# Performance work log

Hardware: AMD Instinct MI355X
Metric: run time of the kernel (lower is better)

The kernel has to match this reference:

```python
import jax, jax.numpy as jnp
import numpy as np

GROUP = 8
BN_SCALE = 1.0 / np.sqrt(1.0 + 1e-5)  # BatchNorm eval with running_mean=0, running_var=1


def _grid_sample(img, grid, align_corners, zeros_pad):
    """Bilinear grid_sample. img: [B,C,H,W]; grid: [B,Hg,Wg,2] in [-1,1]."""
    B, C, H, W = img.shape
    gx, gy = grid[..., 0], grid[..., 1]
    if align_corners:
        ix = (gx + 1.0) * 0.5 * (W - 1)
        iy = (gy + 1.0) * 0.5 * (H - 1)
    else:
        ix = ((gx + 1.0) * W - 1.0) * 0.5
        iy = ((gy + 1.0) * H - 1.0) * 0.5
    x0 = jnp.floor(ix)
    y0 = jnp.floor(iy)
    wx1 = ix - x0
    wy1 = iy - y0
    flat = img.reshape(B, C, H * W)

    def tap(xi, yi, w):
        if zeros_pad:
            valid = (xi >= 0) & (xi <= W - 1) & (yi >= 0) & (yi <= H - 1)
            w = w * valid.astype(img.dtype)
        else:
            xi = jnp.clip(xi, 0, W - 1)
            yi = jnp.clip(yi, 0, H - 1)
        xc = jnp.clip(xi, 0, W - 1).astype(jnp.int32)
        yc = jnp.clip(yi, 0, H - 1).astype(jnp.int32)
        idx = (yc * W + xc).reshape(B, -1)  # [B, Hg*Wg]
        v = jax.vmap(lambda im, ii: jnp.take(im, ii, axis=1))(flat, idx)  # [B,C,Hg*Wg]
        return v.reshape(B, C, gx.shape[1], gx.shape[2]) * w[:, None]

    return (tap(x0, y0, (1.0 - wx1) * (1.0 - wy1))
            + tap(x0 + 1.0, y0, wx1 * (1.0 - wy1))
            + tap(x0, y0 + 1.0, (1.0 - wx1) * wy1)
            + tap(x0 + 1.0, y0 + 1.0, wx1 * wy1))


def _warp(src_fea, src_proj, ref_proj, depth):
    """differentiable_warping: src_fea [B,C,H,W], projs [B,4,4], depth [B,D,H,W] -> [B,C,D,H,W]."""
    B, C, H, W = src_fea.shape
    D = depth.shape[1]
    proj = src_proj @ jnp.linalg.inv(ref_proj)
    rot = proj[:, :3, :3]
    trans = proj[:, :3, 3:4]
    yy, xx = jnp.meshgrid(jnp.arange(H, dtype=jnp.float32), jnp.arange(W, dtype=jnp.float32), indexing='ij')
    xyz = jnp.stack([xx.ravel(), yy.ravel(), jnp.ones(H * W, jnp.float32)], axis=0)  # [3,HW]
    rot_xyz = jnp.einsum('bij,jn->bin', rot, xyz)  # [B,3,HW]
    proj_xyz = rot_xyz[:, :, None, :] * depth.reshape(B, 1, D, H * W) + trans[:, :, :, None]  # [B,3,D,HW]
    neg = proj_xyz[:, 2] <= 1e-3
    px = jnp.where(neg, float(W), proj_xyz[:, 0])
    py = jnp.where(neg, float(H), proj_xyz[:, 1])
    pz = jnp.where(neg, 1.0, proj_xyz[:, 2])
    gx = px / pz / ((W - 1) / 2.0) - 1.0
    gy = py / pz / ((H - 1) / 2.0) - 1.0
    grid = jnp.stack([gx, gy], axis=-1).reshape(B, D * H, W, 2)
    warped = _grid_sample(src_fea, grid, align_corners=True, zeros_pad=True)  # [B,C,D*H,W]
    return warped.reshape(B, C, D, H, W)


def _cbr(x, w, g, b):
    # 1x1x1 Conv3d (no bias) + BN(eval) + ReLU on [B,Cin,D,H,W]
    y = jnp.einsum('oc,bcdhw->bodhw', w, x)
    y = g[None, :, None, None, None] * (y * BN_SCALE) + b[None, :, None, None, None]
    return jax.nn.relu(y)


def setup_inputs() -> dict:
    key = jax.random.key(0)
    ks = jax.random.split(key, 16)
    B, C, H, W, D, V, NN = 2, 64, 128, 160, 16, 4, 9
    G = GROUP
    ref_feature = jax.random.normal(ks[0], (B, C, H, W), jnp.float32)
    src_features = jax.random.normal(ks[1], (V, B, C, H, W), jnp.float32)
    eye = jnp.broadcast_to(jnp.eye(4, dtype=jnp.float32), (B, 4, 4))
    ref_proj = eye + 0.01 * jax.random.normal(ks[2], (B, 4, 4), jnp.float32)
    src_projs = eye[None] + 0.01 * jax.random.normal(ks[3], (V, B, 4, 4), jnp.float32)
    # depths near 1.0 so near-identity projections keep samples in-image
    depth_sample = jnp.sort(0.5 + jax.random.uniform(ks[4], (B, D, H, W), jnp.float32), axis=1)
    grid = jax.random.uniform(ks[5], (B, NN * H, W, 2), jnp.float32, minval=-1.0, maxval=1.0)
    weight = jax.random.uniform(ks[6], (B, D, NN, H, W), jnp.float32)

    def lin(k, o, i):
        return 0.1 * jax.random.normal(k, (o, i), jnp.float32)

    return {
        'ref_feature': ref_feature, 'src_features': src_features,
        'ref_proj': ref_proj, 'src_projs': src_projs,
        'depth_sample': depth_sample, 'grid': grid, 'weight': weight,
        'pw_w0': lin(ks[7], 16, G), 'pw_g0': jnp.ones(16, jnp.float32), 'pw_b0': jnp.zeros(16, jnp.float32),
        'pw_w1': lin(ks[8], 8, 16), 'pw_g1': jnp.ones(8, jnp.float32), 'pw_b1': jnp.zeros(8, jnp.float32),
        'pw_w2': lin(ks[9], 1, 8), 'pw_c2b': jnp.zeros(1, jnp.float32),
        'sn_w0': lin(ks[10], 16, G), 'sn_g0': jnp.ones(16, jnp.float32), 'sn_b0': jnp.zeros(16, jnp.float32),
        'sn_w1': lin(ks[11], 8, 16), 'sn_g1': jnp.ones(8, jnp.float32), 'sn_b1': jnp.zeros(8, jnp.float32),
        'sn_w2': lin(ks[12], 1, 8), 'sn_c2b': jnp.zeros(1, jnp.float32),
        'is_inverse': 0,
    }


def reference(ref_feature, src_features, ref_proj, src_projs, depth_sample, grid, weight,
              pw_w0, pw_g0, pw_b0, pw_w1, pw_g1, pw_b1, pw_w2, pw_c2b,
              sn_w0, sn_g0, sn_b0, sn_w1, sn_g1, sn_b1, sn_w2, sn_c2b, is_inverse):
    B, C, H, W = ref_feature.shape
    D = depth_sample.shape[1]
    V = src_features.shape[0]
    ref_g = ref_feature.reshape(B, GROUP, C // GROUP, 1, H, W)
    weight_sum = jnp.zeros((B, 1, 1, H, W), jnp.float32)
    similarity_sum = jnp.zeros((B, GROUP, D, H, W), jnp.float32)
    vws = []
    for v in range(V):
        warped = _warp(src_features[v], src_projs[v], ref_proj, depth_sample)
        warped = warped.reshape(B, GROUP, C // GROUP, D, H, W)
        sim = (warped * ref_g).mean(axis=2)  # [B,G,D,H,W]
        # PixelwiseNet (view_weights empty -> compute weights)
        y = _cbr(sim, pw_w0, pw_g0, pw_b0)
        y = _cbr(y, pw_w1, pw_g1, pw_b1)
        y = jnp.einsum('oc,bcdhw->bodhw', pw_w2, y) + pw_c2b[None, :, None, None, None]
        vw = jnp.max(jax.nn.sigmoid(y)[:, 0], axis=1)[:, None]  # [B,1,H,W]
        vws.append(vw)
        similarity_sum = similarity_sum + sim * vw[:, None]
        weight_sum = weight_sum + vw[:, None]
    sim_avg = similarity_sum / weight_sum
    # SimilarityNet
    s = _cbr(sim_avg, sn_w0, sn_g0, sn_b0)
    s = _cbr(s, sn_w1, sn_g1, sn_b1)
    s = (jnp.einsum('oc,bcdhw->bodhw', sn_w2, s) + sn_c2b[None, :, None, None, None])[:, 0]  # [B,D,H,W]
    NN = grid.shape[1] // H
    sam = _grid_sample(s, grid, align_corners=False, zeros_pad=False)  # [B,D,NN*H,W]
    sam = sam.reshape(B, D, NN, H, W)
    agg = jnp.sum(sam * weight, axis=2)  # [B,D,H,W]
    score = jax.nn.softmax(agg, axis=1)  # exp(log_softmax) == softmax
    if is_inverse:
        idxs = jnp.arange(D, dtype=jnp.float32).reshape(1, D, 1, 1)
        di = jnp.sum(idxs * score, axis=1)
        inv_min = 1.0 / depth_sample[:, -1]
        inv_max = 1.0 / depth_sample[:, 0]
        depth = 1.0 / (inv_max + di / (D - 1) * (inv_min - inv_max))
    else:
        depth = jnp.sum(depth_sample * score, axis=1)  # [B,H,W]
    view_weights_new = jax.lax.stop_gradient(jnp.concatenate(vws, axis=1))  # [B,V,H,W]
    return depth, score, view_weights_new
```

## Files before the change

### kernel.cpp

```cpp
#include <hip/hip_runtime.h>
#include <math.h>

#define BB 2
#define CC 64
#define HH 128
#define WW 160
#define DD 16
#define VV 4
#define NNB 9
#define GG 8
#define HWSZ (HH*WW)
#define BNS 0.99999500003749977f

typedef _Float16 half2_t __attribute__((ext_vector_type(2)));

__device__ inline half2_t as_h2(unsigned u){ union { unsigned u; half2_t h; } x; x.u = u; return x.h; }
__device__ inline unsigned as_u(half2_t h){ union { unsigned u; half2_t h; } x; x.h = h; return x.u; }

__device__ inline float dot8h(uint4 a, uint4 r) {
    float s = __builtin_amdgcn_fdot2(as_h2(a.x), as_h2(r.x), 0.f, false);
    s = __builtin_amdgcn_fdot2(as_h2(a.y), as_h2(r.y), s, false);
    s = __builtin_amdgcn_fdot2(as_h2(a.z), as_h2(r.z), s, false);
    s = __builtin_amdgcn_fdot2(as_h2(a.w), as_h2(r.w), s, false);
    return s;
}

__device__ inline void inv4(const float* m, float* o) {
    float inv[16];
    inv[0]  =  m[5]*m[10]*m[15] - m[5]*m[11]*m[14] - m[9]*m[6]*m[15] + m[9]*m[7]*m[14] + m[13]*m[6]*m[11] - m[13]*m[7]*m[10];
    inv[4]  = -m[4]*m[10]*m[15] + m[4]*m[11]*m[14] + m[8]*m[6]*m[15] - m[8]*m[7]*m[14] - m[12]*m[6]*m[11] + m[12]*m[7]*m[10];
    inv[8]  =  m[4]*m[9]*m[15]  - m[4]*m[11]*m[13] - m[8]*m[5]*m[15] + m[8]*m[7]*m[13] + m[12]*m[5]*m[11] - m[12]*m[7]*m[9];
    inv[12] = -m[4]*m[9]*m[14]  + m[4]*m[10]*m[13] + m[8]*m[5]*m[14] - m[8]*m[6]*m[13] - m[12]*m[5]*m[10] + m[12]*m[6]*m[9];
    inv[1]  = -m[1]*m[10]*m[15] + m[1]*m[11]*m[14] + m[9]*m[2]*m[15] - m[9]*m[3]*m[14] - m[13]*m[2]*m[11] + m[13]*m[3]*m[10];
    inv[5]  =  m[0]*m[10]*m[15] - m[0]*m[11]*m[14] - m[8]*m[2]*m[15] + m[8]*m[3]*m[14] + m[12]*m[2]*m[11] - m[12]*m[3]*m[10];
    inv[9]  = -m[0]*m[9]*m[15]  + m[0]*m[11]*m[13] + m[8]*m[1]*m[15] - m[8]*m[3]*m[13] - m[12]*m[1]*m[11] + m[12]*m[3]*m[9];
    inv[13] =  m[0]*m[9]*m[14]  - m[0]*m[10]*m[13] - m[8]*m[1]*m[14] + m[8]*m[2]*m[13] + m[12]*m[1]*m[10] - m[12]*m[2]*m[9];
    inv[2]  =  m[1]*m[6]*m[15]  - m[1]*m[7]*m[14]  - m[5]*m[2]*m[15] + m[5]*m[3]*m[14] + m[13]*m[2]*m[7]  - m[13]*m[3]*m[6];
    inv[6]  = -m[0]*m[6]*m[15]  + m[0]*m[7]*m[14]  + m[4]*m[2]*m[15] - m[4]*m[3]*m[14] - m[12]*m[2]*m[7]  + m[12]*m[3]*m[6];
    inv[10] =  m[0]*m[5]*m[15]  - m[0]*m[7]*m[13]  - m[4]*m[1]*m[15] + m[4]*m[3]*m[13] + m[12]*m[1]*m[7]  - m[12]*m[3]*m[5];
    inv[14] = -m[0]*m[5]*m[14]  + m[0]*m[6]*m[13]  + m[4]*m[1]*m[14] - m[4]*m[2]*m[13] - m[12]*m[1]*m[6]  + m[12]*m[2]*m[5];
    inv[3]  = -m[1]*m[6]*m[11]  + m[1]*m[7]*m[10]  + m[5]*m[2]*m[11] - m[5]*m[3]*m[10] - m[9]*m[2]*m[7]   + m[9]*m[3]*m[6];
    inv[7]  =  m[0]*m[6]*m[11]  - m[0]*m[7]*m[10]  - m[4]*m[2]*m[11] + m[4]*m[3]*m[10] + m[8]*m[2]*m[7]   - m[8]*m[3]*m[6];
    inv[11] = -m[0]*m[5]*m[11]  + m[0]*m[7]*m[9]   + m[4]*m[1]*m[11] - m[4]*m[3]*m[9]  - m[8]*m[1]*m[7]   + m[8]*m[3]*m[5];
    inv[15] =  m[0]*m[5]*m[10]  - m[0]*m[6]*m[9]   - m[4]*m[1]*m[10] + m[4]*m[2]*m[9]  + m[8]*m[1]*m[6]   - m[8]*m[2]*m[5];
    float det = m[0]*inv[0] + m[1]*inv[4] + m[2]*inv[8] + m[3]*inv[12];
    det = 1.0f/det;
    #pragma unroll
    for (int i=0;i<16;++i) o[i] = inv[i]*det;
}

__global__ void prep_k(const float* __restrict__ ref_proj, const float* __restrict__ src_projs,
                       const float* __restrict__ pw_w0, const float* __restrict__ pw_g0, const float* __restrict__ pw_b0,
                       const float* __restrict__ pw_w1, const float* __restrict__ pw_g1, const float* __restrict__ pw_b1,
                       const float* __restrict__ pw_w2, const float* __restrict__ pw_c2b,
                       const float* __restrict__ sn_w0, const float* __restrict__ sn_g0, const float* __restrict__ sn_b0,
                       const float* __restrict__ sn_w1, const float* __restrict__ sn_g1, const float* __restrict__ sn_b1,
                       const float* __restrict__ sn_w2, const float* __restrict__ sn_c2b,
                       float* __restrict__ ws) {
    int t = threadIdx.x;
    if (t < VV*BB) {
        int b = t % BB;
        float Mi[16];
        inv4(ref_proj + b*16, Mi);
        const float* A = src_projs + t*16;
        float P[16];
        #pragma unroll
        for (int i=0;i<4;++i)
            #pragma unroll
            for (int j=0;j<4;++j) {
                float s = 0.f;
                #pragma unroll
                for (int k=0;k<4;++k) s += A[i*4+k]*Mi[k*4+j];
                P[i*4+j] = s;
            }
        float* o = ws + t*12;
        o[0]=P[0]; o[1]=P[1]; o[2]=P[2];
        o[3]=P[4]; o[4]=P[5]; o[5]=P[6];
        o[6]=P[8]; o[7]=P[9]; o[8]=P[10];
        o[9]=P[3]; o[10]=P[7]; o[11]=P[11];
    }
    if (t < 128) {
        ws[96 + t]        = pw_w0[t]*pw_g0[t>>3]*BNS;
        ws[96 + 144 + t]  = pw_w1[t]*pw_g1[t>>4]*BNS;
        ws[385 + t]       = sn_w0[t]*sn_g0[t>>3]*BNS;
        ws[385 + 144 + t] = sn_w1[t]*sn_g1[t>>4]*BNS;
    }
    if (t < 16) { ws[96+128+t]=pw_b0[t]; ws[385+128+t]=sn_b0[t]; }
    if (t < 8)  { ws[96+272+t]=pw_b1[t]; ws[96+280+t]=pw_w2[t];
                  ws[385+272+t]=sn_b1[t]; ws[385+280+t]=sn_w2[t]; }
    if (t == 0) { ws[96+288]=pw_c2b[0]; ws[385+288]=sn_c2b[0]; }
}

__global__ __launch_bounds__(256) void transpose_h_k(const float* __restrict__ src,
                                                     _Float16* __restrict__ dst) {
    __shared__ float tb[64][65];
    int img = blockIdx.y;
    int n0  = blockIdx.x * 64;
    const float* ip = src + (size_t)img*64*HWSZ;
    _Float16*    op = dst + (size_t)img*HWSZ*64;
    int tid = threadIdx.x;
    #pragma unroll
    for (int i=0;i<4;++i) {
        int idx = i*256 + tid;
        int c  = idx >> 4;
        int p4 = idx & 15;
        float4 v = *(const float4*)(ip + (size_t)c*HWSZ + n0 + p4*4);
        tb[c][p4*4+0]=v.x; tb[c][p4*4+1]=v.y; tb[c][p4*4+2]=v.z; tb[c][p4*4+3]=v.w;
    }
    __syncthreads();
    #pragma unroll
    for (int i=0;i<4;++i) {
        int idx = i*256 + tid;
        int n  = idx >> 4;
        int cq = idx & 15;
        half2_t h0 = { (_Float16)tb[cq*4+0][n], (_Float16)tb[cq*4+1][n] };
        half2_t h1 = { (_Float16)tb[cq*4+2][n], (_Float16)tb[cq*4+3][n] };
        uint2 u; u.x = as_u(h0); u.y = as_u(h1);
        *(uint2*)(op + (size_t)(n0+n)*64 + cq*4) = u;
    }
}

__device__ inline float pixnet(const float* __restrict__ Wt, const float* sim) {
    float h0[16];
    #pragma unroll
    for (int o=0;o<16;++o) {
        float a = Wt[128+o];
        #pragma unroll
        for (int c=0;c<8;++c) a += Wt[o*8+c]*sim[c];
        h0[o] = fmaxf(a, 0.f);
    }
    float h1[8];
    #pragma unroll
    for (int o=0;o<8;++o) {
        float a = Wt[272+o];
        #pragma unroll
        for (int c=0;c<16;++c) a += Wt[144+o*16+c]*h0[c];
        h1[o] = fmaxf(a, 0.f);
    }
    float y = Wt[288];
    #pragma unroll
    for (int c=0;c<8;++c) y += Wt[280+c]*h1[c];
    return y;
}

__global__ __launch_bounds__(256) void eval_main_k(const float* __restrict__ ref_f,
                                                   const unsigned* __restrict__ src_u,
                                                   const float* __restrict__ wsc,
                                                   const float* __restrict__ depth_sample,
                                                   float* __restrict__ s_buf,
                                                   float* __restrict__ vw_out) {
    __shared__ __align__(16) unsigned refU[16][36];
    int tid  = threadIdx.x;
    int pixL = tid >> 4;
    int d    = tid & 15;
    int pixG = blockIdx.x*16 + pixL;
    int b  = pixG / HWSZ;
    int hw = pixG % HWSZ;
    {
        int c4 = tid & 15;
        const float* rp = ref_f + (size_t)b*CC*HWSZ + (size_t)(c4*4)*HWSZ + hw;
        float f0 = rp[0];
        float f1 = rp[HWSZ];
        float f2 = rp[2*HWSZ];
        float f3 = rp[3*HWSZ];
        half2_t h0 = { (_Float16)f0, (_Float16)f1 };
        half2_t h1 = { (_Float16)f2, (_Float16)f3 };
        refU[pixL][c4*2+0] = as_u(h0);
        refU[pixL][c4*2+1] = as_u(h1);
    }
    __syncthreads();

    int h  = hw / WW;
    int w  = hw % WW;
    const float* pw = wsc + 96;
    const float* sn = wsc + 385;
    float depth = depth_sample[((size_t)b*DD + d)*HWSZ + hw];
    float xf = (float)w, yf = (float)h;

    float simsum[8];
    #pragma unroll
    for (int g=0; g<8; ++g) simsum[g] = 0.f;
    float wsum = 0.f;

    #pragma unroll
    for (int v=0; v<VV; ++v) {
        const float* pm = wsc + (v*BB + b)*12;
        float rx = pm[0]*xf + pm[1]*yf + pm[2];
        float ry = pm[3]*xf + pm[4]*yf + pm[5];
        float rz = pm[6]*xf + pm[7]*yf + pm[8];
        float px = rx*depth + pm[9];
        float py = ry*depth + pm[10];
        float pz = rz*depth + pm[11];
        if (pz <= 0.001f) { px = (float)WW; py = (float)HH; pz = 1.f; }
        float ix = px/pz, iy = py/pz;
        float x0f = floorf(ix), y0f = floorf(iy);
        float wx1 = ix - x0f, wy1 = iy - y0f;
        float vx0 = (x0f      >= 0.f && x0f      <= (float)(WW-1)) ? 1.f : 0.f;
        float vx1 = (x0f+1.f  >= 0.f && x0f+1.f  <= (float)(WW-1)) ? 1.f : 0.f;
        float vy0 = (y0f      >= 0.f && y0f      <= (float)(HH-1)) ? 1.f : 0.f;
        float vy1 = (y0f+1.f  >= 0.f && y0f+1.f  <= (float)(HH-1)) ? 1.f : 0.f;
        float tw00 = (1.f-wx1)*(1.f-wy1)*vx0*vy0;
        float tw10 = wx1*(1.f-wy1)*vx1*vy0;
        float tw01 = (1.f-wx1)*wy1*vx0*vy1;
        float tw11 = wx1*wy1*vx1*vy1;
        int x0c = (int)fminf(fmaxf(x0f,     0.f), (float)(WW-1));
        int x1c = (int)fminf(fmaxf(x0f+1.f, 0.f), (float)(WW-1));
        int y0c = (int)fminf(fmaxf(y0f,     0.f), (float)(HH-1));
        int y1c = (int)fminf(fmaxf(y0f+1.f, 0.f), (float)(HH-1));

        const unsigned* sp  = src_u + (size_t)(v*BB + b)*HWSZ*32;
        const unsigned* p00 = sp + (size_t)(y0c*WW + x0c)*32;
        const unsigned* p10 = sp + (size_t)(y0c*WW + x1c)*32;
        const unsigned* p01 = sp + (size_t)(y1c*WW + x0c)*32;
        const unsigned* p11 = sp + (size_t)(y1c*WW + x1c)*32;

        float sim[8];
        #pragma unroll
        for (int g=0; g<8; ++g) {
            uint4 R  = *(const uint4*)&refU[pixL][g*4];
            uint4 A  = *(const uint4*)(p00 + g*4);
            uint4 Bv = *(const uint4*)(p10 + g*4);
            uint4 Cv = *(const uint4*)(p01 + g*4);
            uint4 E  = *(const uint4*)(p11 + g*4);
            float d00 = dot8h(A,  R);
            float d10 = dot8h(Bv, R);
            float d01 = dot8h(Cv, R);
            float d11 = dot8h(E,  R);
            sim[g] = 0.125f*(tw00*d00 + tw10*d10 + tw01*d01 + tw11*d11);
        }

        float y = pixnet(pw, sim);
        float sg = 1.f/(1.f + __expf(-y));

        float vw = sg;
        vw = fmaxf(vw, __shfl_xor(vw, 1));
        vw = fmaxf(vw, __shfl_xor(vw, 2));
        vw = fmaxf(vw, __shfl_xor(vw, 4));
        vw = fmaxf(vw, __shfl_xor(vw, 8));

        #pragma unroll
        for (int g=0; g<8; ++g) simsum[g] += sim[g]*vw;
        wsum += vw;
        if (d == 0) vw_out[(size_t)(b*VV + v)*HWSZ + hw] = vw;
    }

    float invw = 1.f/wsum;
    float sa[8];
    #pragma unroll
    for (int g=0; g<8; ++g) sa[g] = simsum[g]*invw;
    float s = pixnet(sn, sa);

    s_buf[(size_t)pixG*DD + d] = s;
}

__global__ __launch_bounds__(256) void eval_out_k(const float* __restrict__ s_buf,
                                                  const float* __restrict__ grid,
                                                  const float* __restrict__ weight,
                                                  const float* __restrict__ depth_sample,
                                                  const int* __restrict__ is_inverse,
                                                  float* __restrict__ out) {
    __shared__ float part[4][64][17];
    int tid = threadIdx.x;
    int px  = tid & 63;
    int j   = tid >> 6;
    int t   = blockIdx.x*64 + px;
    int b  = t / HWSZ;
    int hw = t % HWSZ;
    int h  = hw / WW;
    int w  = hw % WW;

    float agg[DD];
    #pragma unroll
    for (int d=0; d<DD; ++d) agg[d] = 0.f;

    #pragma unroll
    for (int k=0; k<3; ++k) {
        int nn = j + k*4;
        if (nn < NNB) {
            const float* gp = grid + (((size_t)b*NNB*HH + nn*HH + h)*WW + w)*2;
            float gx = gp[0], gy = gp[1];
            float ix = ((gx+1.f)*WW - 1.f)*0.5f;
            float iy = ((gy+1.f)*HH - 1.f)*0.5f;
            float x0f = floorf(ix), y0f = floorf(iy);
            float wx1 = ix - x0f, wy1 = iy - y0f;
            int x0 = (int)x0f, y0 = (int)y0f;
            int x0c = x0 < 0 ? 0 : (x0 > WW-1 ? WW-1 : x0);
            int x1c = x0+1 < 0 ? 0 : (x0+1 > WW-1 ? WW-1 : x0+1);
            int y0c = y0 < 0 ? 0 : (y0 > HH-1 ? HH-1 : y0);
            int y1c = y0+1 < 0 ? 0 : (y0+1 > HH-1 ? HH-1 : y0+1);
            float w00 = (1.f-wx1)*(1.f-wy1), w10 = wx1*(1.f-wy1);
            float w01 = (1.f-wx1)*wy1,       w11 = wx1*wy1;
            const float* p00 = s_buf + ((size_t)b*HWSZ + y0c*WW + x0c)*DD;
            const float* p10 = s_buf + ((size_t)b*HWSZ + y0c*WW + x1c)*DD;
            const float* p01 = s_buf + ((size_t)b*HWSZ + y1c*WW + x0c)*DD;
            const float* p11 = s_buf + ((size_t)b*HWSZ + y1c*WW + x1c)*DD;
            const float* wp  = weight + ((size_t)b*DD*NNB + nn)*HWSZ + hw;
            #pragma unroll
            for (int q=0; q<4; ++q) {
                float4 v00 = *(const float4*)(p00 + q*4);
                float4 v10 = *(const float4*)(p10 + q*4);
                float4 v01 = *(const float4*)(p01 + q*4);
                float4 v11 = *(const float4*)(p11 + q*4);
                float s0 = w00*v00.x + w10*v10.x + w01*v01.x + w11*v11.x;
                float s1 = w00*v00.y + w10*v10.y + w01*v01.y + w11*v11.y;
                float s2 = w00*v00.z + w10*v10.z + w01*v01.z + w11*v11.z;
                float s3 = w00*v00.w + w10*v10.w + w01*v01.w + w11*v11.w;
                agg[q*4+0] += s0 * wp[(size_t)(q*4+0)*NNB*HWSZ];
                agg[q*4+1] += s1 * wp[(size_t)(q*4+1)*NNB*HWSZ];
                agg[q*4+2] += s2 * wp[(size_t)(q*4+2)*NNB*HWSZ];
                agg[q*4+3] += s3 * wp[(size_t)(q*4+3)*NNB*HWSZ];
            }
        }
    }

    #pragma unroll
    for (int d=0; d<DD; ++d) part[j][px][d] = agg[d];
    __syncthreads();
    if (j != 0) return;

    #pragma unroll
    for (int d=0; d<DD; ++d)
        agg[d] = part[0][px][d] + part[1][px][d] + part[2][px][d] + part[3][px][d];

    float m = agg[0];
    #pragma unroll
    for (int d=1; d<DD; ++d) m = fmaxf(m, agg[d]);
    float e[DD], sum = 0.f;
    #pragma unroll
    for (int d=0; d<DD; ++d) { e[d] = __expf(agg[d]-m); sum += e[d]; }
    float inv = 1.f/sum;

    const float* dsp = depth_sample + (size_t)b*DD*HWSZ + hw;
    float* sco = out + BB*HWSZ + (size_t)b*DD*HWSZ + hw;
    float dep = 0.f;
    if (*is_inverse) {
        float di = 0.f;
        #pragma unroll
        for (int d=0; d<DD; ++d) { float sc = e[d]*inv; sco[(size_t)d*HWSZ] = sc; di += (float)d*sc; }
        float invmin = 1.f/dsp[(size_t)(DD-1)*HWSZ];
        float invmax = 1.f/dsp[0];
        dep = 1.f/(invmax + di/(float)(DD-1)*(invmin-invmax));
    } else {
        #pragma unroll
        for (int d=0; d<DD; ++d) { float sc = e[d]*inv; sco[(size_t)d*HWSZ] = sc; dep += dsp[(size_t)d*HWSZ]*sc; }
    }
    out[t] = dep;
}

extern "C" void kernel_launch(void* const* d_in, const int* in_sizes, int n_in,
                              void* d_out, int out_size, void* d_ws, size_t ws_size,
                              hipStream_t stream) {
    const float* ref_feature  = (const float*)d_in[0];
    const float* src_features = (const float*)d_in[1];
    const float* ref_proj     = (const float*)d_in[2];
    const float* src_projs    = (const float*)d_in[3];
    const float* depth_sample = (const float*)d_in[4];
    const float* grid         = (const float*)d_in[5];
    const float* weight       = (const float*)d_in[6];
    const float* pw_w0  = (const float*)d_in[7];
    const float* pw_g0  = (const float*)d_in[8];
    const float* pw_b0  = (const float*)d_in[9];
    const float* pw_w1  = (const float*)d_in[10];
    const float* pw_g1  = (const float*)d_in[11];
    const float* pw_b1  = (const float*)d_in[12];
    const float* pw_w2  = (const float*)d_in[13];
    const float* pw_c2b = (const float*)d_in[14];
    const float* sn_w0  = (const float*)d_in[15];
    const float* sn_g0  = (const float*)d_in[16];
    const float* sn_b0  = (const float*)d_in[17];
    const float* sn_w1  = (const float*)d_in[18];
    const float* sn_g1  = (const float*)d_in[19];
    const float* sn_b1  = (const float*)d_in[20];
    const float* sn_w2  = (const float*)d_in[21];
    const float* sn_c2b = (const float*)d_in[22];
    const int*   is_inverse = (const int*)d_in[23];
    float* out = (float*)d_out;

    float*    ws    = (float*)d_ws;
    _Float16* src_h = (_Float16*)(ws + 1024);
    float*    s_buf = ws + 1024 + ((size_t)VV*BB*HWSZ*64)/2;
    size_t need = (size_t)(1024 + (size_t)VV*BB*HWSZ*32 + (size_t)BB*HWSZ*DD)*sizeof(float);
    if (ws_size < need) return;

    prep_k<<<1, 128, 0, stream>>>(ref_proj, src_projs,
                                  pw_w0, pw_g0, pw_b0, pw_w1, pw_g1, pw_b1, pw_w2, pw_c2b,
                                  sn_w0, sn_g0, sn_b0, sn_w1, sn_g1, sn_b1, sn_w2, sn_c2b,
                                  ws);
    transpose_h_k<<<dim3(HWSZ/64, VV*BB), 256, 0, stream>>>(src_features, src_h);
    eval_main_k<<<(BB*HWSZ)/16, 256, 0, stream>>>(ref_feature, (const unsigned*)src_h, ws,
                                                  depth_sample, s_buf,
                                                  out + BB*HWSZ + BB*DD*HWSZ);
    eval_out_k<<<(BB*HWSZ)/64, 256, 0, stream>>>(s_buf, grid, weight, depth_sample,
                                                 is_inverse, out);
}
```

Before: 253.0 us.

## Run pixel MLPs in packed fp16 dot2 and fold prep kernel into transpose

Both small MLPs (PixelwiseNet and SimilarityNet) now use packed fp16 weights and fdot2 instructions instead of fp32 FMAs. This roughly halves the ALU work in the per-depth, per-view inner loop of the main kernel. The weight-prep and projection setup kernel is merged into the first block of the transpose kernel, which removes one launch. fp32-to-fp16 conversions now use packed round-toward-zero (cvt_pkrtz), which slightly changes rounding and accuracy of the intermediate activations.

```diff
diff --git a/kernel.cpp b/kernel.cpp
--- a/kernel.cpp
+++ b/kernel.cpp
@@ -13,9 +13,13 @@
 #define BNS 0.99999500003749977f
 
 typedef _Float16 half2_t __attribute__((ext_vector_type(2)));
+typedef __fp16   fp16x2 __attribute__((ext_vector_type(2)));
 
 __device__ inline half2_t as_h2(unsigned u){ union { unsigned u; half2_t h; } x; x.u = u; return x.h; }
 __device__ inline unsigned as_u(half2_t h){ union { unsigned u; half2_t h; } x; x.h = h; return x.u; }
+__device__ inline half2_t pkrtz(float a, float b){
+    union { fp16x2 f; half2_t h; } x; x.f = __builtin_amdgcn_cvt_pkrtz(a, b); return x.h;
+}
 
 __device__ inline float dot8h(uint4 a, uint4 r) {
     float s = __builtin_amdgcn_fdot2(as_h2(a.x), as_h2(r.x), 0.f, false);
@@ -23,6 +27,34 @@
     s = __builtin_amdgcn_fdot2(as_h2(a.z), as_h2(r.z), s, false);
     s = __builtin_amdgcn_fdot2(as_h2(a.w), as_h2(r.w), s, false);
     return s;
+}
+
+__device__ inline float pixnet_h(const unsigned* __restrict__ W0, const float* __restrict__ b0,
+                                 const unsigned* __restrict__ W1, const float* __restrict__ b1,
+                                 const float* __restrict__ w2, float b2, const float* sim) {
+    half2_t sh[4];
+    #pragma unroll
+    for (int j=0;j<4;++j) sh[j] = pkrtz(sim[2*j], sim[2*j+1]);
+    float h0[16];
+    #pragma unroll
+    for (int o=0;o<16;++o) {
+        float a = b0[o];
+        #pragma unroll
+        for (int j=0;j<4;++j) a = __builtin_amdgcn_fdot2(sh[j], as_h2(W0[o*4+j]), a, false);
+        h0[o] = fmaxf(a, 0.f);
+    }
+    half2_t hh[8];
+    #pragma unroll
+    for (int j=0;j<8;++j) hh[j] = pkrtz(h0[2*j], h0[2*j+1]);
+    float acc = b2;
+    #pragma unroll
+    for (int o=0;o<8;++o) {
+        float a = b1[o];
+        #pragma unroll
+        for (int j=0;j<8;++j) a = __builtin_amdgcn_fdot2(hh[j], as_h2(W1[o*8+j]), a, false);
+        acc += w2[o]*fmaxf(a, 0.f);
+    }
+    return acc;
 }
 
 __device__ inline void inv4(const float* m, float* o) {
@@ -49,56 +81,65 @@
     for (int i=0;i<16;++i) o[i] = inv[i]*det;
 }
 
-__global__ void prep_k(const float* __restrict__ ref_proj, const float* __restrict__ src_projs,
-                       const float* __restrict__ pw_w0, const float* __restrict__ pw_g0, const float* __restrict__ pw_b0,
-                       const float* __restrict__ pw_w1, const float* __restrict__ pw_g1, const float* __restrict__ pw_b1,
-                       const float* __restrict__ pw_w2, const float* __restrict__ pw_c2b,
-                       const float* __restrict__ sn_w0, const float* __restrict__ sn_g0, const float* __restrict__ sn_b0,
-                       const float* __restrict__ sn_w1, const float* __restrict__ sn_g1, const float* __restrict__ sn_b1,
-                       const float* __restrict__ sn_w2, const float* __restrict__ sn_c2b,
-                       float* __restrict__ ws) {
-    int t = threadIdx.x;
-    if (t < VV*BB) {
-        int b = t % BB;
-        float Mi[16];
-        inv4(ref_proj + b*16, Mi);
-        const float* A = src_projs + t*16;
-        float P[16];
-        #pragma unroll
-        for (int i=0;i<4;++i)
+__global__ __launch_bounds__(256) void transpose_h_k(const float* __restrict__ src,
+                                                     _Float16* __restrict__ dst,
+                                                     const float* __restrict__ ref_proj,
+                                                     const float* __restrict__ src_projs,
+                                                     const float* __restrict__ pw_w0, const float* __restrict__ pw_g0, const float* __restrict__ pw_b0,
+                                                     const float* __restrict__ pw_w1, const float* __restrict__ pw_g1, const float* __restrict__ pw_b1,
+                                                     const float* __restrict__ pw_w2, const float* __restrict__ pw_c2b,
+                                                     const float* __restrict__ sn_w0, const float* __restrict__ sn_g0, const float* __restrict__ sn_b0,
+                                                     const float* __restrict__ sn_w1, const float* __restrict__ sn_g1, const float* __restrict__ sn_b1,
+                                                     const float* __restrict__ sn_w2, const float* __restrict__ sn_c2b,
+                                                     float* __restrict__ ws) {
+    int tid = threadIdx.x;
+    if (blockIdx.x == 0 && blockIdx.y == 0) {
+        unsigned* wsu = (unsigned*)ws;
+        int t = tid;
+        if (t < VV*BB) {
+            int b = t % BB;
+            float Mi[16];
+            inv4(ref_proj + b*16, Mi);
+            const float* A = src_projs + t*16;
+            float P[16];
             #pragma unroll
-            for (int j=0;j<4;++j) {
-                float s = 0.f;
+            for (int i=0;i<4;++i)
                 #pragma unroll
-                for (int k=0;k<4;++k) s += A[i*4+k]*Mi[k*4+j];
-                P[i*4+j] = s;
-            }
-        float* o = ws + t*12;
-        o[0]=P[0]; o[1]=P[1]; o[2]=P[2];
-        o[3]=P[4]; o[4]=P[5]; o[5]=P[6];
-        o[6]=P[8]; o[7]=P[9]; o[8]=P[10];
-        o[9]=P[3]; o[10]=P[7]; o[11]=P[11];
-    }
-    if (t < 128) {
-        ws[96 + t]        = pw_w0[t]*pw_g0[t>>3]*BNS;
-        ws[96 + 144 + t]  = pw_w1[t]*pw_g1[t>>4]*BNS;
-        ws[385 + t]       = sn_w0[t]*sn_g0[t>>3]*BNS;
-        ws[385 + 144 + t] = sn_w1[t]*sn_g1[t>>4]*BNS;
-    }
-    if (t < 16) { ws[96+128+t]=pw_b0[t]; ws[385+128+t]=sn_b0[t]; }
-    if (t < 8)  { ws[96+272+t]=pw_b1[t]; ws[96+280+t]=pw_w2[t];
-                  ws[385+272+t]=sn_b1[t]; ws[385+280+t]=sn_w2[t]; }
-    if (t == 0) { ws[96+288]=pw_c2b[0]; ws[385+288]=sn_c2b[0]; }
-}
-
-__global__ __launch_bounds__(256) void transpose_h_k(const float* __restrict__ src,
-                                                     _Float16* __restrict__ dst) {
+                for (int j=0;j<4;++j) {
+                    float s = 0.f;
+                    #pragma unroll
+                    for (int k=0;k<4;++k) s += A[i*4+k]*Mi[k*4+j];
+                    P[i*4+j] = s;
+                }
+            float* o = ws + t*12;
+            o[0]=P[0]; o[1]=P[1]; o[2]=P[2];
+            o[3]=P[4]; o[4]=P[5]; o[5]=P[6];
+            o[6]=P[8]; o[7]=P[9]; o[8]=P[10];
+            o[9]=P[3]; o[10]=P[7]; o[11]=P[11];
+        }
+        if (t < 64) {
+            int o0 = t>>2, j0 = t&3;
+            float g0p = pw_g0[o0]*BNS;
+            wsu[96+t]  = as_u(pkrtz(pw_w0[o0*8+2*j0]*g0p,   pw_w0[o0*8+2*j0+1]*g0p));
+            float g0s = sn_g0[o0]*BNS;
+            wsu[272+t] = as_u(pkrtz(sn_w0[o0*8+2*j0]*g0s,   sn_w0[o0*8+2*j0+1]*g0s));
+            int o1 = t>>3, j1 = t&7;
+            float g1p = pw_g1[o1]*BNS;
+            wsu[176+t] = as_u(pkrtz(pw_w1[o1*16+2*j1]*g1p,  pw_w1[o1*16+2*j1+1]*g1p));
+            float g1s = sn_g1[o1]*BNS;
+            wsu[352+t] = as_u(pkrtz(sn_w1[o1*16+2*j1]*g1s,  sn_w1[o1*16+2*j1+1]*g1s));
+        }
+        if (t < 16) { ws[160+t]=pw_b0[t]; ws[336+t]=sn_b0[t]; }
+        if (t < 8)  { ws[240+t]=pw_b1[t]; ws[248+t]=pw_w2[t];
+                      ws[416+t]=sn_b1[t]; ws[424+t]=sn_w2[t]; }
+        if (t == 0) { ws[256]=pw_c2b[0]; ws[432]=sn_c2b[0]; }
+    }
+
     __shared__ float tb[64][65];
     int img = blockIdx.y;
     int n0  = blockIdx.x * 64;
     const float* ip = src + (size_t)img*64*HWSZ;
     _Float16*    op = dst + (size_t)img*HWSZ*64;
-    int tid = threadIdx.x;
     #pragma unroll
     for (int i=0;i<4;++i) {
         int idx = i*256 + tid;
@@ -113,34 +154,11 @@
         int idx = i*256 + tid;
         int n  = idx >> 4;
         int cq = idx & 15;
-        half2_t h0 = { (_Float16)tb[cq*4+0][n], (_Float16)tb[cq*4+1][n] };
-        half2_t h1 = { (_Float16)tb[cq*4+2][n], (_Float16)tb[cq*4+3][n] };
-        uint2 u; u.x = as_u(h0); u.y = as_u(h1);
+        uint2 u;
+        u.x = as_u(pkrtz(tb[cq*4+0][n], tb[cq*4+1][n]));
+        u.y = as_u(pkrtz(tb[cq*4+2][n], tb[cq*4+3][n]));
         *(uint2*)(op + (size_t)(n0+n)*64 + cq*4) = u;
     }
-}
-
-__device__ inline float pixnet(const float* __restrict__ Wt, const float* sim) {
-    float h0[16];
-    #pragma unroll
-    for (int o=0;o<16;++o) {
-        float a = Wt[128+o];
-        #pragma unroll
-        for (int c=0;c<8;++c) a += Wt[o*8+c]*sim[c];
-        h0[o] = fmaxf(a, 0.f);
-    }
-    float h1[8];
-    #pragma unroll
-    for (int o=0;o<8;++o) {
-        float a = Wt[272+o];
-        #pragma unroll
-        for (int c=0;c<16;++c) a += Wt[144+o*16+c]*h0[c];
-        h1[o] = fmaxf(a, 0.f);
-    }
-    float y = Wt[288];
-    #pragma unroll
-    for (int c=0;c<8;++c) y += Wt[280+c]*h1[c];
-    return y;
 }
 
 __global__ __launch_bounds__(256) void eval_main_k(const float* __restrict__ ref_f,
@@ -163,17 +181,14 @@
         float f1 = rp[HWSZ];
         float f2 = rp[2*HWSZ];
         float f3 = rp[3*HWSZ];
-        half2_t h0 = { (_Float16)f0, (_Float16)f1 };
-        half2_t h1 = { (_Float16)f2, (_Float16)f3 };
-        refU[pixL][c4*2+0] = as_u(h0);
-        refU[pixL][c4*2+1] = as_u(h1);
+        refU[pixL][c4*2+0] = as_u(pkrtz(f0, f1));
+        refU[pixL][c4*2+1] = as_u(pkrtz(f2, f3));
     }
     __syncthreads();
 
     int h  = hw / WW;
     int w  = hw % WW;
-    const float* pw = wsc + 96;
-    const float* sn = wsc + 385;
+    const unsigned* wsu = (const unsigned*)wsc;
     float depth = depth_sample[((size_t)b*DD + d)*HWSZ + hw];
     float xf = (float)w, yf = (float)h;
 
@@ -229,7 +244,7 @@
             sim[g] = 0.125f*(tw00*d00 + tw10*d10 + tw01*d01 + tw11*d11);
         }
 
-        float y = pixnet(pw, sim);
+        float y = pixnet_h(wsu+96, wsc+160, wsu+176, wsc+240, wsc+248, wsc[256], sim);
         float sg = 1.f/(1.f + __expf(-y));
 
         float vw = sg;
@@ -248,7 +263,7 @@
     float sa[8];
     #pragma unroll
     for (int g=0; g<8; ++g) sa[g] = simsum[g]*invw;
-    float s = pixnet(sn, sa);
+    float s = pixnet_h(wsu+272, wsc+336, wsu+352, wsc+416, wsc+424, wsc[432], sa);
 
     s_buf[(size_t)pixG*DD + d] = s;
 }
@@ -382,11 +397,11 @@
     size_t need = (size_t)(1024 + (size_t)VV*BB*HWSZ*32 + (size_t)BB*HWSZ*DD)*sizeof(float);
     if (ws_size < need) return;
 
-    prep_k<<<1, 128, 0, stream>>>(ref_proj, src_projs,
-                                  pw_w0, pw_g0, pw_b0, pw_w1, pw_g1, pw_b1, pw_w2, pw_c2b,
-                                  sn_w0, sn_g0, sn_b0, sn_w1, sn_g1, sn_b1, sn_w2, sn_c2b,
-                                  ws);
-    transpose_h_k<<<dim3(HWSZ/64, VV*BB), 256, 0, stream>>>(src_features, src_h);
+    transpose_h_k<<<dim3(HWSZ/64, VV*BB), 256, 0, stream>>>(src_features, src_h,
+                                                            ref_proj, src_projs,
+                                                            pw_w0, pw_g0, pw_b0, pw_w1, pw_g1, pw_b1, pw_w2, pw_c2b,
+                                                            sn_w0, sn_g0, sn_b0, sn_w1, sn_g1, sn_b1, sn_w2, sn_c2b,
+                                                            ws);
     eval_main_k<<<(BB*HWSZ)/16, 256, 0, stream>>>(ref_feature, (const unsigned*)src_h, ws,
                                                   depth_sample, s_buf,
                                                   out + BB*HWSZ + BB*DD*HWSZ);
```

Result: faster. 236.0 us (-6.7%).
